# Performance work log

Measured on AMD Instinct MI355X. Metric: run time of the kernel, lower is better.

## Reference

```python
import jax, jax.numpy as jnp
import numpy as np

N = 20000      # nodes
E = 320000     # edges
IN = 300       # input_channel
HID = 100      # hidden_channel (= heads*out_channels with heads=1)
R = 50         # num_relations
B = 8          # num_bases (the 4th positional arg 'heads'=8 lands on num_bases in PyG RGATConv)
HEADS = 1
CLS = 3
Q = 64         # number of query (aspect) nodes
EPS = 1e-16


def setup_inputs() -> dict:
    key = jax.random.key(0)
    ks = jax.random.split(key, 16)
    x = jax.random.normal(ks[0], (N, IN), jnp.float32)
    edge_index = jax.random.randint(ks[1], (2, E), 0, N)
    edge_type = jax.random.randint(ks[2], (E,), 0, R)
    query_indices = jax.random.randint(ks[3], (Q,), 0, N)

    def w(k, shape, scale):
        return jax.random.normal(k, shape, jnp.float32) * scale

    comp1 = w(ks[4], (R, B), 0.3)
    basis1 = w(ks[5], (B, IN, HEADS * HID), 1.0 / np.sqrt(IN))
    q1 = w(ks[6], (HEADS * HID, HEADS), 0.1)
    k1 = w(ks[7], (HEADS * HID, HEADS), 0.1)
    b1 = jnp.zeros((HEADS * HID,), jnp.float32)
    comp2 = w(ks[8], (R, B), 0.3)
    basis2 = w(ks[9], (B, HID, HEADS * HID), 1.0 / np.sqrt(HID))
    q2 = w(ks[10], (HEADS * HID, HEADS), 0.1)
    k2 = w(ks[11], (HEADS * HID, HEADS), 0.1)
    b2 = jnp.zeros((HEADS * HID,), jnp.float32)
    Wl = w(ks[12], (CLS, HID), 1.0 / np.sqrt(HID))
    bl = jnp.zeros((CLS,), jnp.float32)
    return dict(x=x, edge_index=edge_index, edge_type=edge_type,
                query_indices=query_indices,
                comp1=comp1, basis1=basis1, q1=q1, k1=k1, b1=b1,
                comp2=comp2, basis2=basis2, q2=q2, k2=k2, b2=b2,
                Wl=Wl, bl=bl)


def segment_softmax(alpha, seg, num_segments):
    # numerically-stable softmax over edges grouped by destination node
    m = jax.ops.segment_max(alpha, seg, num_segments=num_segments)  # [N, H]
    e = jnp.exp(alpha - m[seg])
    s = jax.ops.segment_sum(e, seg, num_segments=num_segments)
    return e / (s[seg] + EPS)


def rgat_conv(x, edge_index, edge_type, comp, basis, q, k, b):
    # basis-decomposed per-relation weight: [R, in, H*out]
    W = jnp.einsum('rb,bio->rio', comp, basis)
    # transform every node under every relation once, then gather per edge
    xt = jnp.einsum('ni,rio->nro', x, W)          # [N, R, H*out]
    src, dst = edge_index[0], edge_index[1]        # j -> i (source_to_target)
    xi = xt[dst, edge_type]                        # [E, H*out]
    xj = xt[src, edge_type]                        # [E, H*out]
    qi = xi @ q                                    # [E, H]
    kj = xj @ k                                    # [E, H]
    alpha = jax.nn.leaky_relu(qi + kj, 0.2)        # additive self-attention
    alpha = segment_softmax(alpha, dst, N)         # across-relation softmax
    msg = xj.reshape(E, HEADS, HID) * alpha[:, :, None]
    out = jax.ops.segment_sum(msg, dst, num_segments=N)  # [N, H, out]
    return out.reshape(N, HEADS * HID) + b         # concat=True


def reference(x, edge_index, edge_type, query_indices,
              comp1, basis1, q1, k1, b1,
              comp2, basis2, q2, k2, b2, Wl, bl):
    h = jax.nn.relu(rgat_conv(x, edge_index, edge_type, comp1, basis1, q1, k1, b1))
    h = jax.nn.relu(rgat_conv(h, edge_index, edge_type, comp2, basis2, q2, k2, b2))
    pooled = h[query_indices].mean(axis=0)          # [HID]
    return pooled @ Wl.T + bl                       # [CLS]
```

## Files before the change

kernel.cpp:

```cpp
#include <hip/hip_runtime.h>
#include <math.h>

#define N_NODES 20000
#define E_EDGES 320000
#define IN_CH   300
#define HID     100
#define R_REL   50
#define NB      8
#define CLS     3
#define NQ      64
#define OUTW    800
#define ZW      128
#define KP1     320
#define KP2     128
#define MPAD    20224
#define NPAIR   79
#define GEMM_RG 48
#define SCAN_BLKS ((N_NODES + 255) / 256)

typedef unsigned short ushort_t;
typedef __attribute__((ext_vector_type(8))) short     short8;
typedef __attribute__((ext_vector_type(8))) unsigned short ushort8;
typedef __attribute__((ext_vector_type(4))) float     f32x4;
typedef __attribute__((ext_vector_type(2))) float     f32x2;

__device__ __forceinline__ ushort_t f2bf_rne(float f) {
    unsigned u = __float_as_uint(f);
    unsigned r = (u + 0x7fffu + ((u >> 16) & 1u)) >> 16;
    return (ushort_t)r;
}
__device__ __forceinline__ float bf2f(ushort_t u) {
    return __uint_as_float((unsigned)u << 16);
}

__global__ __launch_bounds__(256) void zero_deg2(int* __restrict__ dd,
                                                 int* __restrict__ ds) {
    int i = blockIdx.x * 256 + threadIdx.x;
    if (i < N_NODES) { dd[i] = 0; ds[i] = 0; }
}

__global__ __launch_bounds__(256) void zero_hbA(ushort_t* __restrict__ p) {
    int i = blockIdx.x * 256 + threadIdx.x;
    if (i < MPAD * KP2 / 8) {
        ushort8 z = {};
        *(ushort8*)&p[(size_t)i * 8] = z;
    }
}

__global__ __launch_bounds__(256) void hist2_kernel(
        const int* __restrict__ ei, int* __restrict__ dd,
        int* __restrict__ ds) {
    int e = blockIdx.x * 256 + threadIdx.x;
    if (e < E_EDGES) {
        atomicAdd(&dd[ei[E_EDGES + e]], 1);
        atomicAdd(&ds[ei[e]], 1);
    }
}

__global__ __launch_bounds__(256) void scan1_both(
        const int* __restrict__ deg_d, int* __restrict__ rp_d, int* __restrict__ bsum_d,
        const int* __restrict__ deg_s, int* __restrict__ rp_s, int* __restrict__ bsum_s) {
    int set = blockIdx.x / SCAN_BLKS, blk = blockIdx.x % SCAN_BLKS;
    const int* deg = set ? deg_s : deg_d;
    int* rowptr    = set ? rp_s  : rp_d;
    int* bsum      = set ? bsum_s : bsum_d;
    __shared__ int s[256];
    int tid = threadIdx.x;
    int idx = blk * 256 + tid;
    int v = (idx < N_NODES) ? deg[idx] : 0;
    s[tid] = v; __syncthreads();
    #pragma unroll
    for (int off = 1; off < 256; off <<= 1) {
        int t = (tid >= off) ? s[tid - off] : 0;
        __syncthreads();
        s[tid] += t;
        __syncthreads();
    }
    if (idx < N_NODES) rowptr[idx] = s[tid] - v;
    if (tid == 255) bsum[blk] = s[255];
}

__global__ __launch_bounds__(128) void scan2_both(
        int* __restrict__ bsum_d, int* __restrict__ rp_d,
        int* __restrict__ bsum_s, int* __restrict__ rp_s) {
    int* bsum   = blockIdx.x ? bsum_s : bsum_d;
    int* rowptr = blockIdx.x ? rp_s   : rp_d;
    __shared__ int s[128];
    int tid = threadIdx.x;
    int v = (tid < SCAN_BLKS) ? bsum[tid] : 0;
    s[tid] = v; __syncthreads();
    #pragma unroll
    for (int off = 1; off < 128; off <<= 1) {
        int t = (tid >= off) ? s[tid - off] : 0;
        __syncthreads();
        s[tid] += t;
        __syncthreads();
    }
    if (tid < SCAN_BLKS) bsum[tid] = s[tid] - v;
    if (tid == 0) rowptr[N_NODES] = E_EDGES;
}

__global__ __launch_bounds__(256) void scan3_both(
        int* __restrict__ rp_d, const int* __restrict__ bsum_d, int* __restrict__ cur_d,
        int* __restrict__ rp_s, const int* __restrict__ bsum_s, int* __restrict__ cur_s) {
    int set = blockIdx.x / SCAN_BLKS, blk = blockIdx.x % SCAN_BLKS;
    int* rowptr      = set ? rp_s   : rp_d;
    const int* bsum  = set ? bsum_s : bsum_d;
    int* cursor      = set ? cur_s  : cur_d;
    int idx = blk * 256 + threadIdx.x;
    if (idx < N_NODES) {
        int v = rowptr[idx] + bsum[blk];
        rowptr[idx] = v;
        cursor[idx] = v;
    }
}

__global__ __launch_bounds__(256) void scatter_both(
        const int* __restrict__ ei, const int* __restrict__ et,
        int* __restrict__ cur_d, int* __restrict__ cur_s,
        int* __restrict__ skey, int* __restrict__ skey_s,
        int* __restrict__ zidx) {
    int e = blockIdx.x * 256 + threadIdx.x;
    if (e >= E_EDGES) return;
    int s = ei[e], d = ei[E_EDGES + e], rt = et[e];
    int p = atomicAdd(&cur_d[d], 1);
    skey[p] = (s << 6) | rt;
    int qp = atomicAdd(&cur_s[s], 1);
    skey_s[qp] = rt;
    zidx[p] = qp;
}

__global__ __launch_bounds__(256) void split_bt_both(
        const float* __restrict__ basis1, ushort_t* __restrict__ Bt1,
        const float* __restrict__ basis2, ushort_t* __restrict__ Bt2) {
    int idx = blockIdx.x * 256 + threadIdx.x;
    const int n1 = OUTW * KP1;
    if (idx < n1) {
        int n = idx / KP1, k = idx - n * KP1;
        int b = n / HID, o = n - b * HID;
        float v = (k < IN_CH) ? basis1[((size_t)b * IN_CH + k) * HID + o] : 0.f;
        Bt1[idx] = f2bf_rne(v);
    } else {
        int i2 = idx - n1;
        if (i2 >= OUTW * KP2) return;
        int n = i2 / KP2, k = i2 - n * KP2;
        int b = n / HID, o = n - b * HID;
        float v = (k < HID) ? basis2[((size_t)b * HID + k) * HID + o] : 0.f;
        Bt2[i2] = f2bf_rne(v);
    }
}

template<int K, int KP, int RELU>
__global__ __launch_bounds__(256) void cvt_pad_bf16(
        const float* __restrict__ in, ushort_t* __restrict__ out, int M) {
    constexpr int CH = KP / 8;
    int idx = blockIdx.x * 256 + threadIdx.x;
    if (idx >= MPAD * CH) return;
    int n = idx / CH, c = idx - n * CH;
    int k = c * 8;
    float v[8];
    if (n < M && k + 8 <= K) {
        float4 f0 = *(const float4*)&in[(size_t)n * K + k];
        float4 f1 = *(const float4*)&in[(size_t)n * K + k + 4];
        v[0]=f0.x; v[1]=f0.y; v[2]=f0.z; v[3]=f0.w;
        v[4]=f1.x; v[5]=f1.y; v[6]=f1.z; v[7]=f1.w;
    } else {
        #pragma unroll
        for (int i = 0; i < 8; i++)
            v[i] = (n < M && k + i < K) ? in[(size_t)n * K + k + i] : 0.f;
    }
    if (RELU) {
        #pragma unroll
        for (int i = 0; i < 8; i++) v[i] = fmaxf(v[i], 0.f);
    }
    ushort8 hv;
    #pragma unroll
    for (int i = 0; i < 8; i++) hv[i] = f2bf_rne(v[i]);
    *(ushort8*)&out[(size_t)n * KP + k] = hv;
}

template<int KP>
__global__ __launch_bounds__(512, 2) void gemm_mfma(
        const ushort_t* __restrict__ Ab, const ushort_t* __restrict__ Bt,
        ushort_t* __restrict__ xbh, int M) {
    constexpr int KSTEPS = KP / 32;
    constexpr int SW = KP + 8;
    constexpr int CH = KP / 8;
    __shared__ ushort_t Bs[80 * SW];
    int tid = threadIdx.x, lane = tid & 63, wave = tid >> 6;
    int ml = lane & 15, quad = lane >> 4;
    int b = blockIdx.x;
    int xcd = b & 7, qq = b >> 3;
    int cb = qq % 10;
    int rg = xcd + 8 * (qq / 10);
    int col0 = cb * 80;

    for (int t = tid; t < 80 * CH; t += 512) {
        int c = t / CH, ch = t - c * CH;
        *(ushort8*)&Bs[c * SW + ch * 8] =
            *(const ushort8*)&Bt[(size_t)(col0 + c) * KP + ch * 8];
    }
    __syncthreads();

    const ushort_t* bb = &Bs[(size_t)ml * SW + quad * 8];

    for (int g = rg; g < NPAIR; g += GEMM_RG) {
        int rbase = g * 256 + wave * 32;
        const ushort_t* ar0 = Ab + (size_t)(rbase + ml) * KP + quad * 8;
        const ushort_t* ar1 = ar0 + (size_t)16 * KP;
        short8 a0[KSTEPS], a1[KSTEPS];
        #pragma unroll
        for (int ks = 0; ks < KSTEPS; ks++) {
            a0[ks] = *(const short8*)(ar0 + ks * 32);
            a1[ks] = *(const short8*)(ar1 + ks * 32);
        }
        f32x4 acc0[5] = {}, acc1[5] = {};
        #pragma unroll
        for (int ks = 0; ks < KSTEPS; ks++) {
            short8 bf[5];
            #pragma unroll
            for (int nt = 0; nt < 5; nt++)
                bf[nt] = *(const short8*)(bb + nt * 16 * SW + ks * 32);
            #pragma unroll
            for (int nt = 0; nt < 5; nt++) {
                acc0[nt] = __builtin_amdgcn_mfma_f32_16x16x32_bf16(
                               a0[ks], bf[nt], acc0[nt], 0, 0, 0);
                acc1[nt] = __builtin_amdgcn_mfma_f32_16x16x32_bf16(
                               a1[ks], bf[nt], acc1[nt], 0, 0, 0);
            }
        }
        #pragma unroll
        for (int nt = 0; nt < 5; nt++) {
            #pragma unroll
            for (int r = 0; r < 4; r++) {
                int g0 = rbase + quad * 4 + r;
                if (g0 < M)
                    xbh[(size_t)g0 * OUTW + col0 + nt * 16 + ml] =
                        f2bf_rne(acc0[nt][r]);
                int g1 = g0 + 16;
                if (g1 < M)
                    xbh[(size_t)g1 * OUTW + col0 + nt * 16 + ml] =
                        f2bf_rne(acc1[nt][r]);
            }
        }
    }
}

__global__ __launch_bounds__(256) void qk3_kernel(
        const ushort_t* __restrict__ xbh, const float* __restrict__ q,
        const float* __restrict__ k, float* __restrict__ xbq,
        float* __restrict__ xbk) {
    __shared__ float sq[HID], sk[HID];
    int tid = threadIdx.x;
    if (tid < HID) { sq[tid] = q[tid]; sk[tid] = k[tid]; }
    __syncthreads();
    int idx = blockIdx.x * 256 + tid;
    if (idx >= N_NODES * NB) return;
    const ushort_t* xr = xbh + (size_t)(idx >> 3) * OUTW + (idx & 7) * HID;
    float aq = 0.f, ak = 0.f;
    #pragma unroll
    for (int c = 0; c < 25; c++) {
        ushort4 v = *(const ushort4*)&xr[c * 4];
        #pragma unroll
        for (int i = 0; i < 4; i++) {
            float f = bf2f(((const ushort_t*)&v)[i]);
            aq = fmaf(f, sq[c * 4 + i], aq);
            ak = fmaf(f, sk[c * 4 + i], ak);
        }
    }
    xbq[idx] = aq;
    xbk[idx] = ak;
}

__global__ __launch_bounds__(256) void compute_z(
        const int* __restrict__ rowptr_s, const int* __restrict__ skey_s,
        const float* __restrict__ comp, const ushort_t* __restrict__ xbh,
        ushort_t* __restrict__ Z) {
    __shared__ float scomp[R_REL * NB];
    int tid = threadIdx.x;
    for (int i = tid; i < R_REL * NB; i += 256) scomp[i] = comp[i];
    __syncthreads();
    int wave = tid >> 6, lane = tid & 63;
    int s = blockIdx.x * 4 + wave;
    if (s >= N_NODES) return;
    int beg = rowptr_s[s], end = rowptr_s[s + 1];
    if (beg == end) return;
    int eg = lane >> 4, c16 = lane & 15;
    int cbase = c16 * 8;
    float xr[NB][8];
    #pragma unroll
    for (int b = 0; b < NB; b++)
        #pragma unroll
        for (int i = 0; i < 8; i++) xr[b][i] = 0.f;
    if (cbase < HID) {
        #pragma unroll
        for (int b = 0; b < NB; b++) {
            const ushort_t* base = xbh + (size_t)s * OUTW + b * HID + cbase;
            ushort4 v0 = *(const ushort4*)base;
            xr[b][0] = bf2f(v0.x); xr[b][1] = bf2f(v0.y);
            xr[b][2] = bf2f(v0.z); xr[b][3] = bf2f(v0.w);
            if (cbase + 8 <= HID) {
                ushort4 v1 = *(const ushort4*)(base + 4);
                xr[b][4] = bf2f(v1.x); xr[b][5] = bf2f(v1.y);
                xr[b][6] = bf2f(v1.z); xr[b][7] = bf2f(v1.w);
            }
        }
    }
    for (int w0 = beg; w0 < end; w0 += 64) {
        int kw = (w0 + lane < end) ? skey_s[w0 + lane] : 0;
        int wend = w0 + 64 < end ? w0 + 64 : end;
        for (int p0 = w0; p0 < wend; p0 += 4) {
            int j = p0 - w0 + eg;
            int rt = __shfl(kw, j) & 63;
            int p = p0 + eg;
            const float* cr = &scomp[rt * NB];
            float z[8] = {};
            #pragma unroll
            for (int b = 0; b < NB; b++) {
                float cb = cr[b];
                #pragma unroll
                for (int i = 0; i < 8; i++) z[i] = fmaf(cb, xr[b][i], z[i]);
            }
            ushort8 zz;
            #pragma unroll
            for (int i = 0; i < 8; i++) zz[i] = f2bf_rne(z[i]);
            if (p < end)
                *(ushort8*)&Z[(size_t)p * ZW + cbase] = zz;
        }
    }
}

template<int WB>
__global__ __launch_bounds__(256) void msg_soft(
        const int* __restrict__ rowptr, const int* __restrict__ skey,
        const int* __restrict__ zidx,
        const float* __restrict__ comp, const ushort_t* __restrict__ Z,
        const float* __restrict__ xbq, const float* __restrict__ xbk,
        const float* __restrict__ bias, float* __restrict__ h,
        ushort_t* __restrict__ hb) {
    __shared__ float scomp[R_REL * NB];
    int tid = threadIdx.x;
    for (int i = tid; i < R_REL * NB; i += 256) scomp[i] = comp[i];
    __syncthreads();
    int wave = tid >> 6, lane = tid & 63;
    int d = blockIdx.x * 4 + wave;
    if (d >= N_NODES) return;
    int beg = rowptr[d], end = rowptr[d + 1];

    float4 qd0 = *(const float4*)&xbq[d * NB];
    float4 qd1 = *(const float4*)&xbq[d * NB + 4];

    int l5 = lane & 31;
    bool act = l5 < 25;
    int oc = l5 * 4;
    f32x4 acc = {0.f, 0.f, 0.f, 0.f};
    float m = -1e30f, l = 0.f;

    for (int c0 = beg; c0 < end; c0 += 64) {
        int p = c0 + lane;
        bool valid = p < end;
        float a = -1e30f;
        int zi = 0;
        if (valid) {
            int key = skey[p];
            zi = zidx[p];
            int s = key >> 6, rt = key & 63;
            const float4 c0v = *(const float4*)&scomp[rt * NB];
            const float4 c1v = *(const float4*)&scomp[rt * NB + 4];
            const float4 k0v = *(const float4*)&xbk[s * NB];
            const float4 k1v = *(const float4*)&xbk[s * NB + 4];
            float qi = c0v.x*qd0.x + c0v.y*qd0.y + c0v.z*qd0.z + c0v.w*qd0.w
                     + c1v.x*qd1.x + c1v.y*qd1.y + c1v.z*qd1.z + c1v.w*qd1.w;
            float kj = c0v.x*k0v.x + c0v.y*k0v.y + c0v.z*k0v.z + c0v.w*k0v.w
                     + c1v.x*k1v.x + c1v.y*k1v.y + c1v.z*k1v.z + c1v.w*k1v.w;
            float av = qi + kj;
            a = av > 0.f ? av : 0.2f * av;
        }
        float cm = a;
        #pragma unroll
        for (int off = 32; off; off >>= 1) cm = fmaxf(cm, __shfl_xor(cm, off));
        float M = fmaxf(m, cm);
        float scale = __expf(m - M);
        acc *= scale; l *= scale; m = M;
        float wgt = valid ? __expf(a - M) : 0.f;
        float cs = wgt;
        #pragma unroll
        for (int off = 32; off; off >>= 1) cs += __shfl_xor(cs, off);
        l += cs;
        int cnt = end - c0; if (cnt > 64) cnt = 64;
        for (int j = 0; j < cnt; j += 2) {
            int jj = j + (lane >> 5);
            float wj = __shfl(wgt, jj);
            int   zj = __shfl(zi, jj);
            if (act) {
                ushort4 zz = *(const ushort4*)&Z[(size_t)zj * ZW + oc];
                acc.x = fmaf(wj, bf2f(zz.x), acc.x);
                acc.y = fmaf(wj, bf2f(zz.y), acc.y);
                acc.z = fmaf(wj, bf2f(zz.z), acc.z);
                acc.w = fmaf(wj, bf2f(zz.w), acc.w);
            }
        }
    }
    #pragma unroll
    for (int i = 0; i < 4; i++) acc[i] += __shfl_xor(acc[i], 32);
    if (lane < 25) {
        float inv = 1.f / (l + 1e-16f);
        float4 r;
        r.x = bias[oc]     + acc.x * inv;
        r.y = bias[oc + 1] + acc.y * inv;
        r.z = bias[oc + 2] + acc.z * inv;
        r.w = bias[oc + 3] + acc.w * inv;
        if (WB) {
            ushort4 o;
            o.x = f2bf_rne(fmaxf(r.x, 0.f));
            o.y = f2bf_rne(fmaxf(r.y, 0.f));
            o.z = f2bf_rne(fmaxf(r.z, 0.f));
            o.w = f2bf_rne(fmaxf(r.w, 0.f));
            *(ushort4*)&hb[(size_t)d * KP2 + oc] = o;
        } else {
            *(float4*)&h[(size_t)d * HID + oc] = r;
        }
    }
}

__global__ __launch_bounds__(128) void head_kernel(
        const float* __restrict__ h2, const int* __restrict__ qidx,
        const float* __restrict__ Wl, const float* __restrict__ bl,
        float* __restrict__ out) {
    __shared__ float pooled[HID];
    int tid = threadIdx.x;
    if (tid < HID) {
        float s = 0.f;
        for (int i = 0; i < NQ; i++)
            s += fmaxf(h2[(size_t)qidx[i] * HID + tid], 0.f);
        pooled[tid] = s * (1.0f / NQ);
    }
    __syncthreads();
    if (tid < CLS) {
        float s = bl[tid];
        for (int o = 0; o < HID; o++) s = fmaf(pooled[o], Wl[tid * HID + o], s);
        out[tid] = s;
    }
}

extern "C" void kernel_launch(void* const* d_in, const int* in_sizes, int n_in,
                              void* d_out, int out_size, void* d_ws, size_t ws_size,
                              hipStream_t stream) {
    const float* x      = (const float*)d_in[0];
    const int*   ei     = (const int*)  d_in[1];
    const int*   et     = (const int*)  d_in[2];
    const int*   qidx   = (const int*)  d_in[3];
    const float* comp1  = (const float*)d_in[4];
    const float* basis1 = (const float*)d_in[5];
    const float* q1     = (const float*)d_in[6];
    const float* k1     = (const float*)d_in[7];
    const float* b1     = (const float*)d_in[8];
    const float* comp2  = (const float*)d_in[9];
    const float* basis2 = (const float*)d_in[10];
    const float* q2     = (const float*)d_in[11];
    const float* k2     = (const float*)d_in[12];
    const float* b2     = (const float*)d_in[13];
    const float* Wl     = (const float*)d_in[14];
    const float* bl     = (const float*)d_in[15];
    float* out = (float*)d_out;

    char* w = (char*)d_ws;
    size_t off = 0;
    auto alloc = [&](size_t nbytes) {
        void* p = (void*)(w + off);
        off += ((nbytes + 255) / 256) * 256;
        return p;
    };
    ushort_t* xbh    = (ushort_t*)alloc((size_t)N_NODES * OUTW * 2);
    ushort_t* Z      = (ushort_t*)alloc((size_t)E_EDGES * ZW * 2);
    float*    h2     = (float*)alloc((size_t)N_NODES * HID * 4);
    ushort_t* Bt1    = (ushort_t*)alloc((size_t)OUTW * KP1 * 2);
    ushort_t* Bt2    = (ushort_t*)alloc((size_t)OUTW * KP2 * 2);
    ushort_t* xbA    = (ushort_t*)alloc((size_t)MPAD * KP1 * 2);
    ushort_t* hbA    = (ushort_t*)alloc((size_t)MPAD * KP2 * 2);
    float*    xbq    = (float*)alloc((size_t)N_NODES * NB * 4);
    float*    xbk    = (float*)alloc((size_t)N_NODES * NB * 4);
    int*      deg_d  = (int*)alloc(N_NODES * 4);
    int*      deg_s  = (int*)alloc(N_NODES * 4);
    int*      rp_d   = (int*)alloc((N_NODES + 1) * 4);
    int*      rp_s   = (int*)alloc((N_NODES + 1) * 4);
    int*      cur_d  = (int*)alloc(N_NODES * 4);
    int*      cur_s  = (int*)alloc(N_NODES * 4);
    int*      bsum_d = (int*)alloc(SCAN_BLKS * 4);
    int*      bsum_s = (int*)alloc(SCAN_BLKS * 4);
    int*      skey   = (int*)alloc(E_EDGES * 4);
    int*      skey_s = (int*)alloc(E_EDGES * 4);
    int*      zidx   = (int*)alloc(E_EDGES * 4);

    zero_deg2<<<SCAN_BLKS, 256, 0, stream>>>(deg_d, deg_s);
    zero_hbA<<<(MPAD * KP2 / 8 + 255) / 256, 256, 0, stream>>>(hbA);
    hist2_kernel<<<(E_EDGES + 255) / 256, 256, 0, stream>>>(ei, deg_d, deg_s);
    scan1_both<<<2 * SCAN_BLKS, 256, 0, stream>>>(deg_d, rp_d, bsum_d, deg_s, rp_s, bsum_s);
    scan2_both<<<2, 128, 0, stream>>>(bsum_d, rp_d, bsum_s, rp_s);
    scan3_both<<<2 * SCAN_BLKS, 256, 0, stream>>>(rp_d, bsum_d, cur_d, rp_s, bsum_s, cur_s);
    scatter_both<<<(E_EDGES + 255) / 256, 256, 0, stream>>>(ei, et, cur_d, cur_s, skey, skey_s, zidx);
    split_bt_both<<<(OUTW * (KP1 + KP2) + 255) / 256, 256, 0, stream>>>(basis1, Bt1, basis2, Bt2);
    cvt_pad_bf16<IN_CH, KP1, 0><<<(MPAD * (KP1 / 8) + 255) / 256, 256, 0, stream>>>(x, xbA, N_NODES);

    gemm_mfma<KP1><<<10 * GEMM_RG, 512, 0, stream>>>(xbA, Bt1, xbh, N_NODES);
    qk3_kernel<<<(N_NODES * NB + 255) / 256, 256, 0, stream>>>(xbh, q1, k1, xbq, xbk);
    compute_z<<<(N_NODES + 3) / 4, 256, 0, stream>>>(rp_s, skey_s, comp1, xbh, Z);
    msg_soft<1><<<(N_NODES + 3) / 4, 256, 0, stream>>>(rp_d, skey, zidx, comp1, Z, xbq, xbk, b1, (float*)nullptr, hbA);

    gemm_mfma<KP2><<<10 * GEMM_RG, 512, 0, stream>>>(hbA, Bt2, xbh, N_NODES);
    qk3_kernel<<<(N_NODES * NB + 255) / 256, 256, 0, stream>>>(xbh, q2, k2, xbq, xbk);
    compute_z<<<(N_NODES + 3) / 4, 256, 0, stream>>>(rp_s, skey_s, comp2, xbh, Z);
    msg_soft<0><<<(N_NODES + 3) / 4, 256, 0, stream>>>(rp_d, skey, zidx, comp2, Z, xbq, xbk, b2, h2, (ushort_t*)nullptr);

    head_kernel<<<1, 128, 0, stream>>>(h2, qidx, Wl, bl, out);
}
```

Baseline: 378.9 us.

## Fuse q/k projection into GEMM epilogue, merge prep kernels, shrink Z width

Computes the per-basis q/k dot products inside the MFMA GEMM epilogue using cross-lane shuffles. Each 80-column tile writes partial sums into a 16-slot per-node buffer, and msg_soft adds the pairs back together. This drops the separate qk3 kernel and its re-read of xbh. The basis split, x conversion, hbA zeroing and degree zeroing are folded into one prep kernel. The Z row width shrinks from 128 to 104 to cut edge-buffer traffic, and the GEMM launch bound is raised to 4 blocks per CU. The costs are more epilogue work and register pressure in the GEMM, plus extra loads in msg_soft to sum the partials.

```diff
diff --git a/kernel.cpp b/kernel.cpp
--- a/kernel.cpp
+++ b/kernel.cpp
@@ -10,7 +10,7 @@
 #define CLS     3
 #define NQ      64
 #define OUTW    800
-#define ZW      128
+#define ZW      104
 #define KP1     320
 #define KP2     128
 #define MPAD    20224
@@ -31,20 +31,6 @@
 }
 __device__ __forceinline__ float bf2f(ushort_t u) {
     return __uint_as_float((unsigned)u << 16);
-}
-
-__global__ __launch_bounds__(256) void zero_deg2(int* __restrict__ dd,
-                                                 int* __restrict__ ds) {
-    int i = blockIdx.x * 256 + threadIdx.x;
-    if (i < N_NODES) { dd[i] = 0; ds[i] = 0; }
-}
-
-__global__ __launch_bounds__(256) void zero_hbA(ushort_t* __restrict__ p) {
-    int i = blockIdx.x * 256 + threadIdx.x;
-    if (i < MPAD * KP2 / 8) {
-        ushort8 z = {};
-        *(ushort8*)&p[(size_t)i * 8] = z;
-    }
 }
 
 __global__ __launch_bounds__(256) void hist2_kernel(
@@ -130,63 +116,76 @@
     zidx[p] = qp;
 }
 
-__global__ __launch_bounds__(256) void split_bt_both(
+#define PREP_N1 (OUTW * KP1)
+#define PREP_N2 (OUTW * KP2)
+#define PREP_NC (MPAD * (KP1 / 8))
+#define PREP_NZ (MPAD * (KP2 / 8))
+#define PREP_TOT (PREP_N1 + PREP_N2 + PREP_NC + PREP_NZ + N_NODES)
+__global__ __launch_bounds__(256) void prep_kernel(
         const float* __restrict__ basis1, ushort_t* __restrict__ Bt1,
-        const float* __restrict__ basis2, ushort_t* __restrict__ Bt2) {
+        const float* __restrict__ basis2, ushort_t* __restrict__ Bt2,
+        const float* __restrict__ x, ushort_t* __restrict__ xbA,
+        ushort_t* __restrict__ hbA,
+        int* __restrict__ dd, int* __restrict__ ds) {
     int idx = blockIdx.x * 256 + threadIdx.x;
-    const int n1 = OUTW * KP1;
-    if (idx < n1) {
+    if (idx < PREP_N1) {
         int n = idx / KP1, k = idx - n * KP1;
         int b = n / HID, o = n - b * HID;
         float v = (k < IN_CH) ? basis1[((size_t)b * IN_CH + k) * HID + o] : 0.f;
         Bt1[idx] = f2bf_rne(v);
-    } else {
-        int i2 = idx - n1;
-        if (i2 >= OUTW * KP2) return;
-        int n = i2 / KP2, k = i2 - n * KP2;
+        return;
+    }
+    idx -= PREP_N1;
+    if (idx < PREP_N2) {
+        int n = idx / KP2, k = idx - n * KP2;
         int b = n / HID, o = n - b * HID;
         float v = (k < HID) ? basis2[((size_t)b * HID + k) * HID + o] : 0.f;
-        Bt2[i2] = f2bf_rne(v);
-    }
-}
-
-template<int K, int KP, int RELU>
-__global__ __launch_bounds__(256) void cvt_pad_bf16(
-        const float* __restrict__ in, ushort_t* __restrict__ out, int M) {
-    constexpr int CH = KP / 8;
-    int idx = blockIdx.x * 256 + threadIdx.x;
-    if (idx >= MPAD * CH) return;
-    int n = idx / CH, c = idx - n * CH;
-    int k = c * 8;
-    float v[8];
-    if (n < M && k + 8 <= K) {
-        float4 f0 = *(const float4*)&in[(size_t)n * K + k];
-        float4 f1 = *(const float4*)&in[(size_t)n * K + k + 4];
-        v[0]=f0.x; v[1]=f0.y; v[2]=f0.z; v[3]=f0.w;
-        v[4]=f1.x; v[5]=f1.y; v[6]=f1.z; v[7]=f1.w;
-    } else {
-        #pragma unroll
-        for (int i = 0; i < 8; i++)
-            v[i] = (n < M && k + i < K) ? in[(size_t)n * K + k + i] : 0.f;
-    }
-    if (RELU) {
-        #pragma unroll
-        for (int i = 0; i < 8; i++) v[i] = fmaxf(v[i], 0.f);
-    }
-    ushort8 hv;
-    #pragma unroll
-    for (int i = 0; i < 8; i++) hv[i] = f2bf_rne(v[i]);
-    *(ushort8*)&out[(size_t)n * KP + k] = hv;
+        Bt2[idx] = f2bf_rne(v);
+        return;
+    }
+    idx -= PREP_N2;
+    if (idx < PREP_NC) {
+        constexpr int CH = KP1 / 8;
+        int n = idx / CH, c = idx - n * CH;
+        int k = c * 8;
+        float v[8];
+        if (n < N_NODES && k + 8 <= IN_CH) {
+            float4 f0 = *(const float4*)&x[(size_t)n * IN_CH + k];
+            float4 f1 = *(const float4*)&x[(size_t)n * IN_CH + k + 4];
+            v[0]=f0.x; v[1]=f0.y; v[2]=f0.z; v[3]=f0.w;
+            v[4]=f1.x; v[5]=f1.y; v[6]=f1.z; v[7]=f1.w;
+        } else {
+            #pragma unroll
+            for (int i = 0; i < 8; i++)
+                v[i] = (n < N_NODES && k + i < IN_CH) ? x[(size_t)n * IN_CH + k + i] : 0.f;
+        }
+        ushort8 hv;
+        #pragma unroll
+        for (int i = 0; i < 8; i++) hv[i] = f2bf_rne(v[i]);
+        *(ushort8*)&xbA[(size_t)n * KP1 + k] = hv;
+        return;
+    }
+    idx -= PREP_NC;
+    if (idx < PREP_NZ) {
+        ushort8 z = {};
+        *(ushort8*)&hbA[(size_t)idx * 8] = z;
+        return;
+    }
+    idx -= PREP_NZ;
+    if (idx < N_NODES) { dd[idx] = 0; ds[idx] = 0; }
 }
 
 template<int KP>
-__global__ __launch_bounds__(512, 2) void gemm_mfma(
+__global__ __launch_bounds__(512, 4) void gemm_mfma(
         const ushort_t* __restrict__ Ab, const ushort_t* __restrict__ Bt,
-        ushort_t* __restrict__ xbh, int M) {
+        ushort_t* __restrict__ xbh, int M,
+        const float* __restrict__ qw, const float* __restrict__ kw,
+        float* __restrict__ xq, float* __restrict__ xk) {
     constexpr int KSTEPS = KP / 32;
     constexpr int SW = KP + 8;
     constexpr int CH = KP / 8;
     __shared__ ushort_t Bs[80 * SW];
+    __shared__ float sqk[2 * HID];
     int tid = threadIdx.x, lane = tid & 63, wave = tid >> 6;
     int ml = lane & 15, quad = lane >> 4;
     int b = blockIdx.x;
@@ -195,6 +194,7 @@
     int rg = xcd + 8 * (qq / 10);
     int col0 = cb * 80;
 
+    if (tid < 2 * HID) sqk[tid] = (tid < HID) ? qw[tid] : kw[tid - HID];
     for (int t = tid; t < 80 * CH; t += 512) {
         int c = t / CH, ch = t - c * CH;
         *(ushort8*)&Bs[c * SW + ch * 8] =
@@ -203,6 +203,20 @@
     __syncthreads();
 
     const ushort_t* bb = &Bs[(size_t)ml * SW + quad * 8];
+
+    int bLo = col0 / 100, bHi = (col0 + 79) / 100;
+    int split = (bHi != bLo) ? bHi * 100 : (col0 + 160);
+    int slotLo = ((bLo * 100) / 80 == cb) ? 0 : 1;
+    int slotHi = ((bHi * 100) / 80 == cb) ? 0 : 1;
+    float qv[5], kv[5];
+    int himask = 0;
+    #pragma unroll
+    for (int nt = 0; nt < 5; nt++) {
+        int c = col0 + nt * 16 + ml;
+        int cm = c % 100;
+        qv[nt] = sqk[cm]; kv[nt] = sqk[100 + cm];
+        if (c >= split) himask |= 1 << nt;
+    }
 
     for (int g = rg; g < NPAIR; g += GEMM_RG) {
         int rbase = g * 256 + wave * 32;
@@ -243,33 +257,43 @@
                         f2bf_rne(acc1[nt][r]);
             }
         }
-    }
-}
-
-__global__ __launch_bounds__(256) void qk3_kernel(
-        const ushort_t* __restrict__ xbh, const float* __restrict__ q,
-        const float* __restrict__ k, float* __restrict__ xbq,
-        float* __restrict__ xbk) {
-    __shared__ float sq[HID], sk[HID];
-    int tid = threadIdx.x;
-    if (tid < HID) { sq[tid] = q[tid]; sk[tid] = k[tid]; }
-    __syncthreads();
-    int idx = blockIdx.x * 256 + tid;
-    if (idx >= N_NODES * NB) return;
-    const ushort_t* xr = xbh + (size_t)(idx >> 3) * OUTW + (idx & 7) * HID;
-    float aq = 0.f, ak = 0.f;
-    #pragma unroll
-    for (int c = 0; c < 25; c++) {
-        ushort4 v = *(const ushort4*)&xr[c * 4];
-        #pragma unroll
-        for (int i = 0; i < 4; i++) {
-            float f = bf2f(((const ushort_t*)&v)[i]);
-            aq = fmaf(f, sq[c * 4 + i], aq);
-            ak = fmaf(f, sk[c * 4 + i], ak);
-        }
-    }
-    xbq[idx] = aq;
-    xbk[idx] = ak;
+        #pragma unroll
+        for (int r = 0; r < 4; r++) {
+            float pqL = 0, pqH = 0, pkL = 0, pkH = 0;
+            float sqL = 0, sqH = 0, skL = 0, skH = 0;
+            #pragma unroll
+            for (int nt = 0; nt < 5; nt++) {
+                float v0 = acc0[nt][r], v1 = acc1[nt][r];
+                if (himask & (1 << nt)) {
+                    pqH = fmaf(v0, qv[nt], pqH); pkH = fmaf(v0, kv[nt], pkH);
+                    sqH = fmaf(v1, qv[nt], sqH); skH = fmaf(v1, kv[nt], skH);
+                } else {
+                    pqL = fmaf(v0, qv[nt], pqL); pkL = fmaf(v0, kv[nt], pkL);
+                    sqL = fmaf(v1, qv[nt], sqL); skL = fmaf(v1, kv[nt], skL);
+                }
+            }
+            #pragma unroll
+            for (int off = 1; off < 16; off <<= 1) {
+                pqL += __shfl_xor(pqL, off); pqH += __shfl_xor(pqH, off);
+                pkL += __shfl_xor(pkL, off); pkH += __shfl_xor(pkH, off);
+                sqL += __shfl_xor(sqL, off); sqH += __shfl_xor(sqH, off);
+                skL += __shfl_xor(skL, off); skH += __shfl_xor(skH, off);
+            }
+            if (ml == 0) {
+                int r0 = rbase + quad * 4 + r, r1 = r0 + 16;
+                int iLo0 = r0 * 16 + bLo * 2 + slotLo;
+                int iLo1 = r1 * 16 + bLo * 2 + slotLo;
+                xq[iLo0] = pqL; xk[iLo0] = pkL;
+                xq[iLo1] = sqL; xk[iLo1] = skL;
+                if (bHi != bLo) {
+                    int iHi0 = r0 * 16 + bHi * 2 + slotHi;
+                    int iHi1 = r1 * 16 + bHi * 2 + slotHi;
+                    xq[iHi0] = pqH; xk[iHi0] = pkH;
+                    xq[iHi1] = sqH; xk[iHi1] = skH;
+                }
+            }
+        }
+    }
 }
 
 __global__ __launch_bounds__(256) void compute_z(
@@ -324,7 +348,7 @@
             ushort8 zz;
             #pragma unroll
             for (int i = 0; i < 8; i++) zz[i] = f2bf_rne(z[i]);
-            if (p < end)
+            if (p < end && cbase < ZW)
                 *(ushort8*)&Z[(size_t)p * ZW + cbase] = zz;
         }
     }
@@ -335,7 +359,7 @@
         const int* __restrict__ rowptr, const int* __restrict__ skey,
         const int* __restrict__ zidx,
         const float* __restrict__ comp, const ushort_t* __restrict__ Z,
-        const float* __restrict__ xbq, const float* __restrict__ xbk,
+        const float* __restrict__ xbqp, const float* __restrict__ xbkp,
         const float* __restrict__ bias, float* __restrict__ h,
         ushort_t* __restrict__ hb) {
     __shared__ float scomp[R_REL * NB];
@@ -347,8 +371,11 @@
     if (d >= N_NODES) return;
     int beg = rowptr[d], end = rowptr[d + 1];
 
-    float4 qd0 = *(const float4*)&xbq[d * NB];
-    float4 qd1 = *(const float4*)&xbq[d * NB + 4];
+    const float* qp = &xbqp[(size_t)d * 16];
+    float4 qa = *(const float4*)qp,       qb = *(const float4*)(qp + 4);
+    float4 qc = *(const float4*)(qp + 8), qe = *(const float4*)(qp + 12);
+    float4 qd0 = { qa.x + qa.y, qa.z + qa.w, qb.x + qb.y, qb.z + qb.w };
+    float4 qd1 = { qc.x + qc.y, qc.z + qc.w, qe.x + qe.y, qe.z + qe.w };
 
     int l5 = lane & 31;
     bool act = l5 < 25;
@@ -367,8 +394,11 @@
             int s = key >> 6, rt = key & 63;
             const float4 c0v = *(const float4*)&scomp[rt * NB];
             const float4 c1v = *(const float4*)&scomp[rt * NB + 4];
-            const float4 k0v = *(const float4*)&xbk[s * NB];
-            const float4 k1v = *(const float4*)&xbk[s * NB + 4];
+            const float* kp = &xbkp[(size_t)s * 16];
+            float4 ka = *(const float4*)kp,       kb = *(const float4*)(kp + 4);
+            float4 kc = *(const float4*)(kp + 8), ke = *(const float4*)(kp + 12);
+            float4 k0v = { ka.x + ka.y, ka.z + ka.w, kb.x + kb.y, kb.z + kb.w };
+            float4 k1v = { kc.x + kc.y, kc.z + kc.w, ke.x + ke.y, ke.z + ke.w };
             float qi = c0v.x*qd0.x + c0v.y*qd0.y + c0v.z*qd0.z + c0v.w*qd0.w
                      + c1v.x*qd1.x + c1v.y*qd1.y + c1v.z*qd1.z + c1v.w*qd1.w;
             float kj = c0v.x*k0v.x + c0v.y*k0v.y + c0v.z*k0v.z + c0v.w*k0v.w
@@ -478,8 +508,8 @@
     ushort_t* Bt2    = (ushort_t*)alloc((size_t)OUTW * KP2 * 2);
     ushort_t* xbA    = (ushort_t*)alloc((size_t)MPAD * KP1 * 2);
     ushort_t* hbA    = (ushort_t*)alloc((size_t)MPAD * KP2 * 2);
-    float*    xbq    = (float*)alloc((size_t)N_NODES * NB * 4);
-    float*    xbk    = (float*)alloc((size_t)N_NODES * NB * 4);
+    float*    xbqp   = (float*)alloc((size_t)MPAD * 16 * 4);
+    float*    xbkp   = (float*)alloc((size_t)MPAD * 16 * 4);
     int*      deg_d  = (int*)alloc(N_NODES * 4);
     int*      deg_s  = (int*)alloc(N_NODES * 4);
     int*      rp_d   = (int*)alloc((N_NODES + 1) * 4);
@@ -492,25 +522,21 @@
     int*      skey_s = (int*)alloc(E_EDGES * 4);
     int*      zidx   = (int*)alloc(E_EDGES * 4);
 
-    zero_deg2<<<SCAN_BLKS, 256, 0, stream>>>(deg_d, deg_s);
-    zero_hbA<<<(MPAD * KP2 / 8 + 255) / 256, 256, 0, stream>>>(hbA);
+    prep_kernel<<<(PREP_TOT + 255) / 256, 256, 0, stream>>>(
+        basis1, Bt1, basis2, Bt2, x, xbA, hbA, deg_d, deg_s);
     hist2_kernel<<<(E_EDGES + 255) / 256, 256, 0, stream>>>(ei, deg_d, deg_s);
     scan1_both<<<2 * SCAN_BLKS, 256, 0, stream>>>(deg_d, rp_d, bsum_d, deg_s, rp_s, bsum_s);
     scan2_both<<<2, 128, 0, stream>>>(bsum_d, rp_d, bsum_s, rp_s);
     scan3_both<<<2 * SCAN_BLKS, 256, 0, stream>>>(rp_d, bsum_d, cur_d, rp_s, bsum_s, cur_s);
     scatter_both<<<(E_EDGES + 255) / 256, 256, 0, stream>>>(ei, et, cur_d, cur_s, skey, skey_s, zidx);
-    split_bt_both<<<(OUTW * (KP1 + KP2) + 255) / 256, 256, 0, stream>>>(basis1, Bt1, basis2, Bt2);
-    cvt_pad_bf16<IN_CH, KP1, 0><<<(MPAD * (KP1 / 8) + 255) / 256, 256, 0, stream>>>(x, xbA, N_NODES);
-
-    gemm_mfma<KP1><<<10 * GEMM_RG, 512, 0, stream>>>(xbA, Bt1, xbh, N_NODES);
-    qk3_kernel<<<(N_NODES * NB + 255) / 256, 256, 0, stream>>>(xbh, q1, k1, xbq, xbk);
+
+    gemm_mfma<KP1><<<10 * GEMM_RG, 512, 0, stream>>>(xbA, Bt1, xbh, N_NODES, q1, k1, xbqp, xbkp);
     compute_z<<<(N_NODES + 3) / 4, 256, 0, stream>>>(rp_s, skey_s, comp1, xbh, Z);
-    msg_soft<1><<<(N_NODES + 3) / 4, 256, 0, stream>>>(rp_d, skey, zidx, comp1, Z, xbq, xbk, b1, (float*)nullptr, hbA);
-
-    gemm_mfma<KP2><<<10 * GEMM_RG, 512, 0, stream>>>(hbA, Bt2, xbh, N_NODES);
-    qk3_kernel<<<(N_NODES * NB + 255) / 256, 256, 0, stream>>>(xbh, q2, k2, xbq, xbk);
+    msg_soft<1><<<(N_NODES + 3) / 4, 256, 0, stream>>>(rp_d, skey, zidx, comp1, Z, xbqp, xbkp, b1, (float*)nullptr, hbA);
+
+    gemm_mfma<KP2><<<10 * GEMM_RG, 512, 0, stream>>>(hbA, Bt2, xbh, N_NODES, q2, k2, xbqp, xbkp);
     compute_z<<<(N_NODES + 3) / 4, 256, 0, stream>>>(rp_s, skey_s, comp2, xbh, Z);
-    msg_soft<0><<<(N_NODES + 3) / 4, 256, 0, stream>>>(rp_d, skey, zidx, comp2, Z, xbq, xbk, b2, h2, (ushort_t*)nullptr);
+    msg_soft<0><<<(N_NODES + 3) / 4, 256, 0, stream>>>(rp_d, skey, zidx, comp2, Z, xbqp, xbkp, b2, h2, (ushort_t*)nullptr);
 
     head_kernel<<<1, 128, 0, stream>>>(h2, qidx, Wl, bl, out);
 }
```

Result: slower. 483.1 us (+27.5%).
